# Optimization experiments

Measured on AMD Instinct MI355X. Metric: run time of the kernel, lower is better.

## Reference

```python
import jax, jax.numpy as jnp
import numpy as np

DIM = 2048
NUM_HEADS = 16
HEAD_DIM = DIM // NUM_HEADS
SCALE = 1.0 / float(np.sqrt(HEAD_DIM))


def setup_inputs() -> dict:
    key = jax.random.key(0)
    ks = jax.random.split(key, 7)
    B, L = 2, 2048
    x = jax.random.normal(ks[0], (B, L, DIM), dtype=jnp.float32)
    s = 1.0 / np.sqrt(DIM)
    # nn.Linear stores weight as [out, in]; y = x @ W.T + b
    Wq = jax.random.uniform(ks[1], (DIM, DIM), jnp.float32, -s, s)
    bq = jax.random.uniform(ks[2], (DIM,), jnp.float32, -s, s)
    Wk = jax.random.uniform(ks[3], (DIM, DIM), jnp.float32, -s, s)
    bk = jax.random.uniform(ks[4], (DIM,), jnp.float32, -s, s)
    Wv = jax.random.uniform(ks[5], (DIM, DIM), jnp.float32, -s, s)
    bv = jax.random.uniform(ks[6], (DIM,), jnp.float32, -s, s)
    return {"x": x, "Wq": Wq, "bq": bq, "Wk": Wk, "bk": bk, "Wv": Wv, "bv": bv}


def _attn(x, Wq, bq, Wk, bk, Wv, bv):
    B, L, D = x.shape
    H, Hd = NUM_HEADS, HEAD_DIM
    # projections: x @ W.T + b, then split heads -> [B, H, L, Hd]
    q = (x @ Wq.T + bq).reshape(B, L, H, Hd).transpose(0, 2, 1, 3)
    k = (x @ Wk.T + bk).reshape(B, L, H, Hd).transpose(0, 2, 1, 3)
    v = (x @ Wv.T + bv).reshape(B, L, H, Hd).transpose(0, 2, 1, 3)
    scores = jnp.einsum("bhqd,bhkd->bhqk", q, k) * SCALE  # [B,H,L,L]
    attn = jax.nn.softmax(scores, axis=-1)
    out = jnp.einsum("bhqk,bhkd->bhqd", attn, v)
    return out.transpose(0, 2, 1, 3).reshape(B, L, D)


def reference(x, Wq, bq, Wk, bk, Wv, bv):
    return _attn(x, Wq, bq, Wk, bk, Wv, bv)
```

## Files before the change

kernel.cpp:

```cpp
#include <hip/hip_runtime.h>
#include <stdint.h>

typedef unsigned short u16;
typedef __attribute__((ext_vector_type(8))) short short8;
typedef __attribute__((ext_vector_type(16))) float f32x16;

#define ATTN_SCALE 0.08838834764831845f

__device__ __forceinline__ u16 f2bf(float f) {
  union { float f; uint32_t u; } a; a.f = f;
  return (u16)((a.u + 0x7fffu + ((a.u >> 16) & 1u)) >> 16);
}

__device__ __forceinline__ void async16(const u16* g, u16* lds) {
  __builtin_amdgcn_global_load_lds(
      (const __attribute__((address_space(1))) void*)g,
      (__attribute__((address_space(3))) void*)lds, 16, 0, 0);
}

__global__ void cvt_kernel(const float* __restrict__ src, u16* __restrict__ dst, int n8) {
  int i = blockIdx.x * 256 + threadIdx.x;
  if (i >= n8) return;
  const float4* s4 = (const float4*)src;
  float4 a = s4[2 * i], c = s4[2 * i + 1];
  union { u16 h[8]; uint4 v; } o;
  o.h[0] = f2bf(a.x); o.h[1] = f2bf(a.y); o.h[2] = f2bf(a.z); o.h[3] = f2bf(a.w);
  o.h[4] = f2bf(c.x); o.h[5] = f2bf(c.y); o.h[6] = f2bf(c.z); o.h[7] = f2bf(c.w);
  ((uint4*)dst)[i] = o.v;
}

__global__ void cvtw_kernel(const float* __restrict__ w0, const float* __restrict__ w1,
                            const float* __restrict__ w2, u16* __restrict__ dst) {
  int z = blockIdx.y;
  const float* src = (z == 0) ? w0 : (z == 1) ? w1 : w2;
  int i = blockIdx.x * 256 + threadIdx.x;
  const float4* s4 = (const float4*)src;
  float4 a = s4[2 * i], c = s4[2 * i + 1];
  union { u16 h[8]; uint4 v; } o;
  o.h[0] = f2bf(a.x); o.h[1] = f2bf(a.y); o.h[2] = f2bf(a.z); o.h[3] = f2bf(a.w);
  o.h[4] = f2bf(c.x); o.h[5] = f2bf(c.y); o.h[6] = f2bf(c.z); o.h[7] = f2bf(c.w);
  ((uint4*)(dst + (size_t)z * 4194304))[i] = o.v;
}

__global__ __launch_bounds__(256, 4) void qkv_gemm(
    const u16* __restrict__ xb, const u16* __restrict__ Wb,
    const float* __restrict__ bq, const float* __restrict__ bk, const float* __restrict__ bv,
    u16* __restrict__ qkv) {
  __shared__ __align__(16) u16 As[2][128 * 32];
  __shared__ __align__(16) u16 Bs[2][128 * 32];
  const int z = blockIdx.z;
  const int n0 = blockIdx.x * 128, m0 = blockIdx.y * 128;
  const u16* Bw = Wb + (size_t)z * (2048u * 2048u);
  const float* bias = (z == 0) ? bq : (z == 1) ? bk : bv;
  u16* dst = qkv + (size_t)z * 8388608u;
  const int t = threadIdx.x, wave = t >> 6, lane = t & 63;
  const int wm = wave >> 1, wn = wave & 1, l31 = lane & 31, h = lane >> 5;

  int soff[2], goff[2];
#pragma unroll
  for (int p = 0; p < 2; ++p) {
    const int s = p * 256 + wave * 64 + lane;
    const int R = s >> 4, j = s & 15, u = j ^ (R & 15);
    const int m = R * 4 + (u >> 2), c = u & 3;
    soff[p] = s * 8;
    goff[p] = m * 2048 + c * 8;
  }
  int fr16[2][2], fR15[2][2];
  const int q4 = (l31 & 3) * 4;
#pragma unroll
  for (int i = 0; i < 2; ++i) {
    const int mA = wm * 64 + i * 32 + l31, mB = wn * 64 + i * 32 + l31;
    fr16[0][i] = (mA >> 2) * 16; fR15[0][i] = (mA >> 2) & 15;
    fr16[1][i] = (mB >> 2) * 16; fR15[1][i] = (mB >> 2) & 15;
  }

  f32x16 acc[2][2];
#pragma unroll
  for (int i = 0; i < 2; ++i)
#pragma unroll
    for (int j = 0; j < 2; ++j)
#pragma unroll
      for (int r = 0; r < 16; ++r) acc[i][j][r] = 0.f;

  const u16* Abase = xb + (size_t)m0 * 2048;
  const u16* Bbase = Bw + (size_t)n0 * 2048;

#pragma unroll 1
  for (int n = 0; n < 64; ++n) {
    if (n == 0) {
#pragma unroll
      for (int p = 0; p < 2; ++p) {
        async16(Abase + goff[p], &As[0][soff[p]]);
        async16(Bbase + goff[p], &Bs[0][soff[p]]);
      }
    }
    __syncthreads();
    const int cur = n & 1;
    if (n + 1 < 64) {
      const int k1 = (n + 1) * 32;
#pragma unroll
      for (int p = 0; p < 2; ++p) {
        async16(Abase + goff[p] + k1, &As[cur ^ 1][soff[p]]);
        async16(Bbase + goff[p] + k1, &Bs[cur ^ 1][soff[p]]);
      }
    }
#pragma unroll
    for (int ks = 0; ks < 2; ++ks) {
      const int c = ks * 2 + h;
      short8 af[2], bf[2];
#pragma unroll
      for (int i = 0; i < 2; ++i) {
        af[i] = *(const short8*)&As[cur][(fr16[0][i] + ((q4 + c) ^ fR15[0][i])) * 8];
        bf[i] = *(const short8*)&Bs[cur][(fr16[1][i] + ((q4 + c) ^ fR15[1][i])) * 8];
      }
#pragma unroll
      for (int i = 0; i < 2; ++i)
#pragma unroll
        for (int j = 0; j < 2; ++j)
          acc[i][j] = __builtin_amdgcn_mfma_f32_32x32x16_bf16(af[i], bf[j], acc[i][j], 0, 0, 0);
    }
  }

#pragma unroll
  for (int j = 0; j < 2; ++j) {
    const int col = n0 + wn * 64 + j * 32 + l31;
    const float bb_ = bias[col];
    const int hh = col >> 7, hd = col & 127;
#pragma unroll
    for (int i = 0; i < 2; ++i) {
#pragma unroll
      for (int g = 0; g < 4; ++g) {
        const int lbase = m0 + wm * 64 + i * 32 + 8 * g + 4 * h;
        const int bb = lbase >> 11, l0 = lbase & 2047;
        if (z == 2) {
          union { u16 q[4]; uint2 d; } pk;
#pragma unroll
          for (int rr = 0; rr < 4; ++rr) pk.q[rr] = f2bf(acc[i][j][4 * g + rr] + bb_);
          *(uint2*)&dst[((size_t)(bb * 16 + hh) * 128 + hd) * 2048 + l0] = pk.d;
        } else {
#pragma unroll
          for (int rr = 0; rr < 4; ++rr)
            dst[((size_t)(bb * 16 + hh) * 2048 + (l0 + rr)) * 128 + hd] =
                f2bf(acc[i][j][4 * g + rr] + bb_);
        }
      }
    }
  }
}

__global__ __launch_bounds__(256, 2) void attn_kernel(
    const u16* __restrict__ Qg,
    const u16* __restrict__ Kg,
    const u16* __restrict__ Vtg,
    float* __restrict__ out) {
  __shared__ __align__(16) u16 Ks[2][64 * 128];
  __shared__ __align__(16) u16 Vs[2][128 * 64];
  const int bh = blockIdx.y, q0 = blockIdx.x * 128;
  const int t = threadIdx.x, wave = t >> 6, lane = t & 63;
  const int l31 = lane & 31, h = lane >> 5;
  const u16* Qp = Qg + (size_t)bh * 262144;
  const u16* Kp = Kg + (size_t)bh * 262144;
  const u16* Vp = Vtg + (size_t)bh * 262144;
  const int b = bh >> 4, hd = bh & 15;
  const int qrow = q0 + wave * 32 + l31;

  short8 qf[8];
#pragma unroll
  for (int s = 0; s < 8; ++s)
    qf[s] = *(const short8*)&Qp[(size_t)qrow * 128 + s * 16 + h * 8];

  int kOff[4], kSlot[4], vOff[4], vSlot[4];
#pragma unroll
  for (int p = 0; p < 4; ++p) {
    const int s = p * 256 + wave * 64 + lane;
    const int rk = s >> 4, gk = (s & 15) ^ (rk & 15);
    kSlot[p] = s * 8; kOff[p] = rk * 128 + gk * 8;
    const int rv = s >> 3, gv = (s & 7) ^ (rv & 7);
    vSlot[p] = s * 8; vOff[p] = rv * 2048 + gv * 8;
  }

  f32x16 oac[4];
#pragma unroll
  for (int dt = 0; dt < 4; ++dt)
#pragma unroll
    for (int r = 0; r < 16; ++r) oac[dt][r] = 0.f;
  float den = 0.f;

#pragma unroll
  for (int p = 0; p < 4; ++p) async16(Kp + kOff[p], &Ks[0][kSlot[p]]);
#pragma unroll
  for (int p = 0; p < 4; ++p) async16(Vp + vOff[p], &Vs[0][vSlot[p]]);

#pragma unroll 1
  for (int kt = 0; kt < 32; ++kt) {
    __syncthreads();
    const int cur = kt & 1;
    if (kt + 1 < 32) {
      const int k1 = (kt + 1) * 64;
#pragma unroll
      for (int p = 0; p < 4; ++p)
        async16(Kp + (size_t)k1 * 128 + kOff[p], &Ks[cur ^ 1][kSlot[p]]);
#pragma unroll
      for (int p = 0; p < 4; ++p)
        async16(Vp + (size_t)k1 + vOff[p], &Vs[cur ^ 1][vSlot[p]]);
    }

#pragma unroll
    for (int T = 0; T < 2; ++T) {
      const int krow = T * 32 + l31;
      f32x16 sc;
#pragma unroll
      for (int r = 0; r < 16; ++r) sc[r] = 0.f;
#pragma unroll
      for (int s = 0; s < 8; ++s) {
        const short8 kf = *(const short8*)&Ks[cur][(krow * 16 + ((2 * s + h) ^ (krow & 15))) * 8];
        sc = __builtin_amdgcn_mfma_f32_32x32x16_bf16(kf, qf[s], sc, 0, 0, 0);
      }
      uint32_t pp[8];
#pragma unroll
      for (int i = 0; i < 8; ++i) {
        const float e0 = __expf(fminf(sc[2 * i] * ATTN_SCALE, 80.f));
        const float e1 = __expf(fminf(sc[2 * i + 1] * ATTN_SCALE, 80.f));
        den += e0 + e1;
        union { float f; uint32_t u; } u0, u1; u0.f = e0; u1.f = e1;
        pp[i] = ((u1.u + 0x8000u) & 0xffff0000u) | ((u0.u + 0x8000u) >> 16);
      }
      uint32_t x[8];
#pragma unroll
      for (int i = 0; i < 8; ++i) x[i] = __shfl_xor(pp[i], 32, 64);
#pragma unroll
      for (int ks = 0; ks < 2; ++ks) {
        const int o0 = ks * 4;
        union { uint32_t u[4]; short8 s8; } bfp;
        bfp.u[0] = h ? x[o0 + 2] : pp[o0 + 0];
        bfp.u[1] = h ? x[o0 + 3] : pp[o0 + 1];
        bfp.u[2] = h ? pp[o0 + 2] : x[o0 + 0];
        bfp.u[3] = h ? pp[o0 + 3] : x[o0 + 1];
        const int gk = T * 4 + ks * 2 + h;
#pragma unroll
        for (int dt = 0; dt < 4; ++dt) {
          const int vrow = dt * 32 + l31;
          const short8 vf = *(const short8*)&Vs[cur][(vrow * 8 + (gk ^ (vrow & 7))) * 8];
          oac[dt] = __builtin_amdgcn_mfma_f32_32x32x16_bf16(vf, bfp.s8, oac[dt], 0, 0, 0);
        }
      }
    }
  }

  den += __shfl_xor(den, 32, 64);
  const float inv = 1.f / den;
#pragma unroll
  for (int dt = 0; dt < 4; ++dt) {
#pragma unroll
    for (int g4 = 0; g4 < 4; ++g4) {
      float4 o;
      o.x = oac[dt][4 * g4 + 0] * inv;
      o.y = oac[dt][4 * g4 + 1] * inv;
      o.z = oac[dt][4 * g4 + 2] * inv;
      o.w = oac[dt][4 * g4 + 3] * inv;
      const int d = dt * 32 + g4 * 8 + h * 4;
      *(float4*)&out[((size_t)(b * 2048 + qrow)) * 2048 + hd * 128 + d] = o;
    }
  }
}

extern "C" void kernel_launch(void* const* d_in, const int* in_sizes, int n_in,
                              void* d_out, int out_size, void* d_ws, size_t ws_size,
                              hipStream_t stream) {
  const float* x  = (const float*)d_in[0];
  const float* Wq = (const float*)d_in[1];
  const float* bq = (const float*)d_in[2];
  const float* Wk = (const float*)d_in[3];
  const float* bk = (const float*)d_in[4];
  const float* Wv = (const float*)d_in[5];
  const float* bv = (const float*)d_in[6];
  float* out = (float*)d_out;
  if (ws_size < 92274688u) return;

  u16* xb  = (u16*)d_ws;
  u16* Wb  = xb + 8388608;
  u16* qkv = Wb + 12582912;

  cvt_kernel<<<4096, 256, 0, stream>>>(x, xb, 1048576);
  cvtw_kernel<<<dim3(2048, 3), 256, 0, stream>>>(Wq, Wk, Wv, Wb);
  qkv_gemm<<<dim3(16, 32, 3), 256, 0, stream>>>(xb, Wb, bq, bk, bv, qkv);
  attn_kernel<<<dim3(16, 32), 256, 0, stream>>>(qkv, qkv + 8388608, qkv + 16777216, out);
}
```

Before: 351.3 us.

## Enlarge QKV GEMM tiles to 256x256 with a 4-stage async LDS pipeline

```diff
diff --git a/kernel.cpp b/kernel.cpp
--- a/kernel.cpp
+++ b/kernel.cpp
@@ -42,106 +42,123 @@
   ((uint4*)(dst + (size_t)z * 4194304))[i] = o.v;
 }
 
-__global__ __launch_bounds__(256, 4) void qkv_gemm(
+__global__ __launch_bounds__(512, 2) void qkv_gemm(
     const u16* __restrict__ xb, const u16* __restrict__ Wb,
     const float* __restrict__ bq, const float* __restrict__ bk, const float* __restrict__ bv,
     u16* __restrict__ qkv) {
-  __shared__ __align__(16) u16 As[2][128 * 32];
-  __shared__ __align__(16) u16 Bs[2][128 * 32];
+  extern __shared__ __align__(16) u16 smem[];
+  u16* As = smem;
+  u16* Bs = smem + 32768;
   const int z = blockIdx.z;
-  const int n0 = blockIdx.x * 128, m0 = blockIdx.y * 128;
-  const u16* Bw = Wb + (size_t)z * (2048u * 2048u);
+  const int n0 = blockIdx.x * 256, m0 = blockIdx.y * 256;
+  const u16* Bw = Wb + (size_t)z * 4194304u;
   const float* bias = (z == 0) ? bq : (z == 1) ? bk : bv;
   u16* dst = qkv + (size_t)z * 8388608u;
-  const int t = threadIdx.x, wave = t >> 6, lane = t & 63;
-  const int wm = wave >> 1, wn = wave & 1, l31 = lane & 31, h = lane >> 5;
+  const int t = threadIdx.x;
+  const int wave = t >> 6, lane = t & 63;
+  const int wm = wave >> 2, wn = wave & 3, l31 = lane & 31, h = lane >> 5;
 
   int soff[2], goff[2];
 #pragma unroll
   for (int p = 0; p < 2; ++p) {
-    const int s = p * 256 + wave * 64 + lane;
+    const int s = p * 512 + t;
     const int R = s >> 4, j = s & 15, u = j ^ (R & 15);
-    const int m = R * 4 + (u >> 2), c = u & 3;
+    const int m = 4 * R + (u >> 2), c = u & 3;
     soff[p] = s * 8;
     goff[p] = m * 2048 + c * 8;
   }
-  int fr16[2][2], fR15[2][2];
   const int q4 = (l31 & 3) * 4;
-#pragma unroll
-  for (int i = 0; i < 2; ++i) {
-    const int mA = wm * 64 + i * 32 + l31, mB = wn * 64 + i * 32 + l31;
-    fr16[0][i] = (mA >> 2) * 16; fR15[0][i] = (mA >> 2) & 15;
-    fr16[1][i] = (mB >> 2) * 16; fR15[1][i] = (mB >> 2) & 15;
-  }
-
-  f32x16 acc[2][2];
-#pragma unroll
-  for (int i = 0; i < 2; ++i)
-#pragma unroll
-    for (int j = 0; j < 2; ++j)
-#pragma unroll
-      for (int r = 0; r < 16; ++r) acc[i][j][r] = 0.f;
+  int fr16A[4], fR15A[4], fr16B[2], fR15B[2];
+#pragma unroll
+  for (int am = 0; am < 4; ++am) {
+    const int mA = wm * 128 + am * 32 + l31;
+    fr16A[am] = (mA >> 2) * 16; fR15A[am] = (mA >> 2) & 15;
+  }
+#pragma unroll
+  for (int bn = 0; bn < 2; ++bn) {
+    const int mB = wn * 64 + bn * 32 + l31;
+    fr16B[bn] = (mB >> 2) * 16; fR15B[bn] = (mB >> 2) & 15;
+  }
+
+  f32x16 acc[4][2];
+#pragma unroll
+  for (int am = 0; am < 4; ++am)
+#pragma unroll
+    for (int bn = 0; bn < 2; ++bn)
+#pragma unroll
+      for (int r = 0; r < 16; ++r) acc[am][bn][r] = 0.f;
 
   const u16* Abase = xb + (size_t)m0 * 2048;
   const u16* Bbase = Bw + (size_t)n0 * 2048;
 
+#pragma unroll
+  for (int r = 0; r < 3; ++r) {
+    const int k0 = r * 32;
+#pragma unroll
+    for (int p = 0; p < 2; ++p) async16(Abase + goff[p] + k0, &As[r * 8192 + soff[p]]);
+#pragma unroll
+    for (int p = 0; p < 2; ++p) async16(Bbase + goff[p] + k0, &Bs[r * 8192 + soff[p]]);
+  }
+
 #pragma unroll 1
-  for (int n = 0; n < 64; ++n) {
-    if (n == 0) {
-#pragma unroll
-      for (int p = 0; p < 2; ++p) {
-        async16(Abase + goff[p], &As[0][soff[p]]);
-        async16(Bbase + goff[p], &Bs[0][soff[p]]);
-      }
-    }
-    __syncthreads();
-    const int cur = n & 1;
-    if (n + 1 < 64) {
-      const int k1 = (n + 1) * 32;
-#pragma unroll
-      for (int p = 0; p < 2; ++p) {
-        async16(Abase + goff[p] + k1, &As[cur ^ 1][soff[p]]);
-        async16(Bbase + goff[p] + k1, &Bs[cur ^ 1][soff[p]]);
-      }
-    }
-#pragma unroll
-    for (int ks = 0; ks < 2; ++ks) {
-      const int c = ks * 2 + h;
-      short8 af[2], bf[2];
-#pragma unroll
-      for (int i = 0; i < 2; ++i) {
-        af[i] = *(const short8*)&As[cur][(fr16[0][i] + ((q4 + c) ^ fR15[0][i])) * 8];
-        bf[i] = *(const short8*)&Bs[cur][(fr16[1][i] + ((q4 + c) ^ fR15[1][i])) * 8];
-      }
-#pragma unroll
-      for (int i = 0; i < 2; ++i)
-#pragma unroll
-        for (int j = 0; j < 2; ++j)
-          acc[i][j] = __builtin_amdgcn_mfma_f32_32x32x16_bf16(af[i], bf[j], acc[i][j], 0, 0, 0);
-    }
-  }
-
-#pragma unroll
-  for (int j = 0; j < 2; ++j) {
-    const int col = n0 + wn * 64 + j * 32 + l31;
+  for (int kt = 0; kt < 64; ++kt) {
+    if (kt <= 61)      asm volatile("s_waitcnt vmcnt(8)" ::: "memory");
+    else if (kt == 62) asm volatile("s_waitcnt vmcnt(4)" ::: "memory");
+    else               asm volatile("s_waitcnt vmcnt(0)" ::: "memory");
+    __builtin_amdgcn_s_barrier();
+    __builtin_amdgcn_sched_barrier(0);
+
+    if (kt + 3 < 64) {
+      const int k0 = (kt + 3) * 32, bn_ = (kt + 3) & 3;
+#pragma unroll
+      for (int p = 0; p < 2; ++p) async16(Abase + goff[p] + k0, &As[bn_ * 8192 + soff[p]]);
+#pragma unroll
+      for (int p = 0; p < 2; ++p) async16(Bbase + goff[p] + k0, &Bs[bn_ * 8192 + soff[p]]);
+    }
+
+    const u16* aL = As + (kt & 3) * 8192;
+    const u16* bL = Bs + (kt & 3) * 8192;
+#pragma unroll
+    for (int kk = 0; kk < 2; ++kk) {
+      const int c = kk * 2 + h;
+      short8 af[4], bf[2];
+#pragma unroll
+      for (int am = 0; am < 4; ++am)
+        af[am] = *(const short8*)&aL[(fr16A[am] + ((q4 + c) ^ fR15A[am])) * 8];
+#pragma unroll
+      for (int bn = 0; bn < 2; ++bn)
+        bf[bn] = *(const short8*)&bL[(fr16B[bn] + ((q4 + c) ^ fR15B[bn])) * 8];
+      __builtin_amdgcn_s_setprio(1);
+#pragma unroll
+      for (int am = 0; am < 4; ++am)
+#pragma unroll
+        for (int bn = 0; bn < 2; ++bn)
+          acc[am][bn] = __builtin_amdgcn_mfma_f32_32x32x16_bf16(af[am], bf[bn], acc[am][bn], 0, 0, 0);
+      __builtin_amdgcn_s_setprio(0);
+    }
+  }
+
+#pragma unroll
+  for (int bn = 0; bn < 2; ++bn) {
+    const int col = n0 + wn * 64 + bn * 32 + l31;
     const float bb_ = bias[col];
     const int hh = col >> 7, hd = col & 127;
 #pragma unroll
-    for (int i = 0; i < 2; ++i) {
+    for (int am = 0; am < 4; ++am) {
 #pragma unroll
       for (int g = 0; g < 4; ++g) {
-        const int lbase = m0 + wm * 64 + i * 32 + 8 * g + 4 * h;
+        const int lbase = m0 + wm * 128 + am * 32 + 8 * g + 4 * h;
         const int bb = lbase >> 11, l0 = lbase & 2047;
         if (z == 2) {
           union { u16 q[4]; uint2 d; } pk;
 #pragma unroll
-          for (int rr = 0; rr < 4; ++rr) pk.q[rr] = f2bf(acc[i][j][4 * g + rr] + bb_);
+          for (int rr = 0; rr < 4; ++rr) pk.q[rr] = f2bf(acc[am][bn][4 * g + rr] + bb_);
           *(uint2*)&dst[((size_t)(bb * 16 + hh) * 128 + hd) * 2048 + l0] = pk.d;
         } else {
 #pragma unroll
           for (int rr = 0; rr < 4; ++rr)
             dst[((size_t)(bb * 16 + hh) * 2048 + (l0 + rr)) * 128 + hd] =
-                f2bf(acc[i][j][4 * g + rr] + bb_);
+                f2bf(acc[am][bn][4 * g + rr] + bb_);
         }
       }
     }
@@ -283,6 +300,6 @@
 
   cvt_kernel<<<4096, 256, 0, stream>>>(x, xb, 1048576);
   cvtw_kernel<<<dim3(2048, 3), 256, 0, stream>>>(Wq, Wk, Wv, Wb);
-  qkv_gemm<<<dim3(16, 32, 3), 256, 0, stream>>>(xb, Wb, bq, bk, bv, qkv);
+  qkv_gemm<<<dim3(8, 16, 3), 512, 131072, stream>>>(xb, Wb, bq, bk, bv, qkv);
   attn_kernel<<<dim3(16, 32), 256, 0, stream>>>(qkv, qkv + 8388608, qkv + 16777216, out);
 }
```

New measurement: 355.3 us. Within noise of the previous version (+1.1%).

## Fuse conversion kernels and use 512-thread attention blocks with swizzled block order

Applied to the files above, without the earlier changes.

```diff
diff --git a/kernel.cpp b/kernel.cpp
--- a/kernel.cpp
+++ b/kernel.cpp
@@ -18,28 +18,24 @@
       (__attribute__((address_space(3))) void*)lds, 16, 0, 0);
 }
 
-__global__ void cvt_kernel(const float* __restrict__ src, u16* __restrict__ dst, int n8) {
-  int i = blockIdx.x * 256 + threadIdx.x;
-  if (i >= n8) return;
+__global__ void cvt_all_kernel(const float* __restrict__ x,
+                               const float* __restrict__ w0, const float* __restrict__ w1,
+                               const float* __restrict__ w2,
+                               u16* __restrict__ xb, u16* __restrict__ Wb) {
+  const int z = blockIdx.y;
+  const float* src; u16* dst; int i;
+  if (z < 2) { src = x;  dst = xb; i = (z * 2048 + blockIdx.x) * 256 + threadIdx.x; }
+  else {
+    src = (z == 2) ? w0 : (z == 3) ? w1 : w2;
+    dst = Wb + (size_t)(z - 2) * 4194304u;
+    i = blockIdx.x * 256 + threadIdx.x;
+  }
   const float4* s4 = (const float4*)src;
   float4 a = s4[2 * i], c = s4[2 * i + 1];
   union { u16 h[8]; uint4 v; } o;
   o.h[0] = f2bf(a.x); o.h[1] = f2bf(a.y); o.h[2] = f2bf(a.z); o.h[3] = f2bf(a.w);
   o.h[4] = f2bf(c.x); o.h[5] = f2bf(c.y); o.h[6] = f2bf(c.z); o.h[7] = f2bf(c.w);
   ((uint4*)dst)[i] = o.v;
-}
-
-__global__ void cvtw_kernel(const float* __restrict__ w0, const float* __restrict__ w1,
-                            const float* __restrict__ w2, u16* __restrict__ dst) {
-  int z = blockIdx.y;
-  const float* src = (z == 0) ? w0 : (z == 1) ? w1 : w2;
-  int i = blockIdx.x * 256 + threadIdx.x;
-  const float4* s4 = (const float4*)src;
-  float4 a = s4[2 * i], c = s4[2 * i + 1];
-  union { u16 h[8]; uint4 v; } o;
-  o.h[0] = f2bf(a.x); o.h[1] = f2bf(a.y); o.h[2] = f2bf(a.z); o.h[3] = f2bf(a.w);
-  o.h[4] = f2bf(c.x); o.h[5] = f2bf(c.y); o.h[6] = f2bf(c.z); o.h[7] = f2bf(c.w);
-  ((uint4*)(dst + (size_t)z * 4194304))[i] = o.v;
 }
 
 __global__ __launch_bounds__(256, 4) void qkv_gemm(
@@ -148,14 +144,16 @@
   }
 }
 
-__global__ __launch_bounds__(256, 2) void attn_kernel(
+__global__ __launch_bounds__(512, 1) void attn_kernel(
     const u16* __restrict__ Qg,
     const u16* __restrict__ Kg,
     const u16* __restrict__ Vtg,
     float* __restrict__ out) {
   __shared__ __align__(16) u16 Ks[2][64 * 128];
   __shared__ __align__(16) u16 Vs[2][128 * 64];
-  const int bh = blockIdx.y, q0 = blockIdx.x * 128;
+  const int s_lin = blockIdx.y * 8 + blockIdx.x;
+  const int w = (s_lin & 7) * 32 + (s_lin >> 3);
+  const int bh = w >> 3, q0 = (w & 7) * 256;
   const int t = threadIdx.x, wave = t >> 6, lane = t & 63;
   const int l31 = lane & 31, h = lane >> 5;
   const u16* Qp = Qg + (size_t)bh * 262144;
@@ -169,10 +167,10 @@
   for (int s = 0; s < 8; ++s)
     qf[s] = *(const short8*)&Qp[(size_t)qrow * 128 + s * 16 + h * 8];
 
-  int kOff[4], kSlot[4], vOff[4], vSlot[4];
-#pragma unroll
-  for (int p = 0; p < 4; ++p) {
-    const int s = p * 256 + wave * 64 + lane;
+  int kOff[2], kSlot[2], vOff[2], vSlot[2];
+#pragma unroll
+  for (int p = 0; p < 2; ++p) {
+    const int s = p * 512 + t;
     const int rk = s >> 4, gk = (s & 15) ^ (rk & 15);
     kSlot[p] = s * 8; kOff[p] = rk * 128 + gk * 8;
     const int rv = s >> 3, gv = (s & 7) ^ (rv & 7);
@@ -187,9 +185,9 @@
   float den = 0.f;
 
 #pragma unroll
-  for (int p = 0; p < 4; ++p) async16(Kp + kOff[p], &Ks[0][kSlot[p]]);
-#pragma unroll
-  for (int p = 0; p < 4; ++p) async16(Vp + vOff[p], &Vs[0][vSlot[p]]);
+  for (int p = 0; p < 2; ++p) async16(Kp + kOff[p], &Ks[0][kSlot[p]]);
+#pragma unroll
+  for (int p = 0; p < 2; ++p) async16(Vp + vOff[p], &Vs[0][vSlot[p]]);
 
 #pragma unroll 1
   for (int kt = 0; kt < 32; ++kt) {
@@ -198,10 +196,10 @@
     if (kt + 1 < 32) {
       const int k1 = (kt + 1) * 64;
 #pragma unroll
-      for (int p = 0; p < 4; ++p)
+      for (int p = 0; p < 2; ++p)
         async16(Kp + (size_t)k1 * 128 + kOff[p], &Ks[cur ^ 1][kSlot[p]]);
 #pragma unroll
-      for (int p = 0; p < 4; ++p)
+      for (int p = 0; p < 2; ++p)
         async16(Vp + (size_t)k1 + vOff[p], &Vs[cur ^ 1][vSlot[p]]);
     }
 
@@ -281,8 +279,7 @@
   u16* Wb  = xb + 8388608;
   u16* qkv = Wb + 12582912;
 
-  cvt_kernel<<<4096, 256, 0, stream>>>(x, xb, 1048576);
-  cvtw_kernel<<<dim3(2048, 3), 256, 0, stream>>>(Wq, Wk, Wv, Wb);
+  cvt_all_kernel<<<dim3(2048, 5), 256, 0, stream>>>(x, Wq, Wk, Wv, xb, Wb);
   qkv_gemm<<<dim3(16, 32, 3), 256, 0, stream>>>(xb, Wb, bq, bk, bv, qkv);
-  attn_kernel<<<dim3(16, 32), 256, 0, stream>>>(qkv, qkv + 8388608, qkv + 16777216, out);
-}
+  attn_kernel<<<dim3(8, 32), 512, 0, stream>>>(qkv, qkv + 8388608, qkv + 16777216, out);
+}
```

New measurement: 353.8 us. No clear change (+0.7%).
